# Performance work log

Measured on AMD Instinct MI355X. Metric: run time of the kernel, lower is better.

## Reference

```python
import math
import jax, jax.numpy as jnp
import numpy as np

NGRAM = 2
NUM_HEADS = 16
EMBED_DIM = 1024
HEAD_DIM = EMBED_DIM // NUM_HEADS
NUM_BUCKETS = 32
MAX_DIST = 128
REAL_T = 512
BSZ = 4
NEG = -10000.0


def _bucket_np(n):
    # unidirectional T5-style log bucket, matching _relative_positions_bucket
    n = np.maximum(n, 0)
    max_exact = NUM_BUCKETS // 2
    is_small = n < max_exact
    val = max_exact + np.log(np.maximum(n, 1) / max_exact) / math.log(MAX_DIST / max_exact) * (NUM_BUCKETS - max_exact)
    val = np.minimum(val, NUM_BUCKETS - 1).astype(np.int32)
    return np.where(is_small, n.astype(np.int32), val)


def setup_inputs() -> dict:
    key = jax.random.key(0)
    ks = jax.random.split(key, 4)
    T, B, E = REAL_T, BSZ, EMBED_DIM
    hidden_states = jax.random.normal(ks[0], ((1 + NGRAM) * T, B, E), jnp.float32)
    s = 1.0 / math.sqrt(E)  # ~xavier scale
    in_proj_weight = jax.random.uniform(ks[1], (3 * E, E), jnp.float32, -s, s)
    in_proj_bias = jnp.zeros((3 * E,), jnp.float32)
    rel_w = jax.random.uniform(ks[2], (NUM_BUCKETS * NUM_HEADS, E), jnp.float32, -s, s)
    rel_b = jnp.zeros((NUM_BUCKETS * NUM_HEADS,), jnp.float32)
    out_w = jax.random.uniform(ks[3], (E, E), jnp.float32, -s, s)
    out_b = jnp.zeros((E,), jnp.float32)
    # relative-position buckets (main stream: keys at positions 1..T)
    pos = np.arange(1, T + 1)
    i_buckets_main = np.broadcast_to(_bucket_np(pos[:, None] - pos[None, :]), (B, T, T)).copy()
    # predict stream keys: concat(main positions shifted by -1, predict positions)
    key_pos = np.concatenate([pos - 1, pos])
    i_buckets_ngram = np.broadcast_to(_bucket_np(pos[:, None] - key_pos[None, :]), (B, T, 2 * T)).copy()
    # masks
    t = np.arange(T)
    self_attn_mask = np.where(t[None, :] <= t[:, None], 0.0, NEG).astype(np.float32)  # causal [T,T]
    s_idx = np.arange(2 * T)
    allow = ((s_idx[None, :] < T) & (s_idx[None, :] <= t[:, None])) | (s_idx[None, :] == T + t[:, None])
    ngram_mask = np.broadcast_to(np.where(allow, 0.0, NEG).astype(np.float32), (NGRAM, T, 2 * T)).copy()
    return dict(
        hidden_states=hidden_states,
        in_proj_weight=in_proj_weight, in_proj_bias=in_proj_bias,
        rel_w=rel_w, rel_b=rel_b, out_w=out_w, out_b=out_b,
        self_attn_mask=jnp.asarray(self_attn_mask), ngram_mask=jnp.asarray(ngram_mask),
        i_buckets_main=jnp.asarray(i_buckets_main, jnp.int32),
        i_buckets_ngram=jnp.asarray(i_buckets_ngram, jnp.int32),
    )


def _rel_values(h, rel_w, rel_b):
    # h: [..., T, E] -> per-head bucket values [..., H, T, NUM_BUCKETS]
    vals = h @ rel_w.T + rel_b                              # [..., T, K*H]
    vals = vals.reshape(vals.shape[:-1] + (NUM_BUCKETS, NUM_HEADS))  # [..., T, K, H]
    return jnp.moveaxis(vals, (-1, -2), (-3, -1))           # [..., H, T, K]


def _forward(hidden_states, in_proj_weight, in_proj_bias, rel_w, rel_b, out_w, out_b,
             self_attn_mask, ngram_mask, i_buckets_main, i_buckets_ngram):
    tgt_len, B, E = hidden_states.shape
    T = tgt_len // (1 + NGRAM)
    H, d = NUM_HEADS, HEAD_DIM
    scaling = d ** -0.5

    qkv = hidden_states @ in_proj_weight.T + in_proj_bias
    q, k, v = jnp.split(qkv, 3, axis=-1)
    q = q * scaling

    def to_bh(x):  # [tgt_len, B, E] -> [B*H, tgt_len, d]
        return jnp.swapaxes(x.reshape(tgt_len, B * H, d), 0, 1)

    q, k, v = to_bh(q), to_bh(k), to_bh(v)
    q_main, k_main, v_main = q[:, :T], k[:, :T], v[:, :T]

    # ---- main stream ----
    aw_main = jnp.einsum('btd,bsd->bts', q_main, k_main)            # [BH,T,T]
    h_main = jnp.swapaxes(hidden_states[:T], 0, 1)                  # [B,T,E]
    vals_main = _rel_values(h_main, rel_w, rel_b)                   # [B,H,T,K]
    idx = jnp.broadcast_to(i_buckets_main[:, None], (B, H, T, T))
    rel_main = jnp.take_along_axis(vals_main, idx, axis=-1).reshape(B * H, T, T)
    aw_main = aw_main + rel_main + self_attn_mask[None]
    p_main = jax.nn.softmax(aw_main.astype(jnp.float32), axis=-1).astype(aw_main.dtype)
    attn_main = jnp.einsum('bts,bsd->btd', p_main, v_main)          # [BH,T,d]
    attn_main = jnp.swapaxes(attn_main, 0, 1).reshape(T, B, E) @ out_w.T + out_b

    # ---- ngram (predict) streams ----
    S2 = 2 * T
    q_ng = jnp.moveaxis(q[:, T:].reshape(B * H, NGRAM, T, d), 1, 0)  # [N,BH,T,d]
    k_ng = jnp.moveaxis(k[:, T:].reshape(B * H, NGRAM, T, d), 1, 0)
    v_ng = jnp.moveaxis(v[:, T:].reshape(B * H, NGRAM, T, d), 1, 0)
    k_cat = jnp.concatenate([jnp.broadcast_to(k_main[None], (NGRAM, B * H, T, d)), k_ng], axis=2)  # [N,BH,2T,d]
    v_cat = jnp.concatenate([jnp.broadcast_to(v_main[None], (NGRAM, B * H, T, d)), v_ng], axis=2)
    aw_ng = jnp.einsum('nbtd,nbsd->nbts', q_ng, k_cat)               # [N,BH,T,2T]
    h_ng = jnp.swapaxes(hidden_states[T:].reshape(NGRAM, T, B, E), 1, 2)  # [N,B,T,E]
    vals_ng = _rel_values(h_ng, rel_w, rel_b)                        # [N,B,H,T,K]
    idx2 = jnp.broadcast_to(i_buckets_ngram[None, :, None], (NGRAM, B, H, T, S2))
    rel_ng = jnp.take_along_axis(vals_ng, idx2, axis=-1).reshape(NGRAM, B * H, T, S2)
    aw_ng = aw_ng + rel_ng + ngram_mask[:, None]
    p_ng = jax.nn.softmax(aw_ng.astype(jnp.float32), axis=-1).astype(aw_ng.dtype)
    attn_ng = jnp.einsum('nbts,nbsd->nbtd', p_ng, v_cat)             # [N,BH,T,d]
    attn_ng = jnp.swapaxes(attn_ng, 1, 2).reshape(NGRAM, T, B, E) @ out_w.T + out_b

    return jnp.concatenate([attn_main, attn_ng.reshape(NGRAM * T, B, E)], axis=0)  # [(1+N)T,B,E]


def reference(hidden_states, in_proj_weight, in_proj_bias, rel_w, rel_b, out_w, out_b,
              self_attn_mask, ngram_mask, i_buckets_main, i_buckets_ngram):
    return _forward(hidden_states, in_proj_weight, in_proj_bias, rel_w, rel_b, out_w, out_b,
                    self_attn_mask, ngram_mask, i_buckets_main, i_buckets_ngram)
```

## Files before the change

kernel.cpp:

```cpp
#include <hip/hip_runtime.h>
#include <stdint.h>

#define T_LEN 512
#define NTOK  1536
#define EMB   1024
#define BS    4

typedef __bf16 bf16x8 __attribute__((ext_vector_type(8)));
typedef float  f32x4  __attribute__((ext_vector_type(4)));

__device__ __forceinline__ float bflo(unsigned short u){
  union { unsigned int i; float f; } a; a.i = ((unsigned int)u) << 16; return a.f;
}
__device__ __forceinline__ unsigned short f2bf(float f){
  union { float f; unsigned int i; } v; v.f = f;
  unsigned int x = v.i;
  return (unsigned short)((x + 0x7fffu + ((x >> 16) & 1u)) >> 16);
}

__device__ __forceinline__ void gld_lds16(const unsigned short* gptr, unsigned short* lptr){
  __builtin_amdgcn_global_load_lds(
      (const __attribute__((address_space(1))) unsigned int*)gptr,
      (__attribute__((address_space(3))) unsigned int*)lptr, 16, 0, 0);
}

__global__ __launch_bounds__(256)
void cast_k(const float* __restrict__ h, const float* __restrict__ wq,
            const float* __restrict__ rw, const float* __restrict__ ow,
            unsigned short* __restrict__ Hb, unsigned short* __restrict__ Wc,
            unsigned short* __restrict__ Ob)
{
  const size_t e = ((size_t)blockIdx.x * 256 + threadIdx.x) * 8;
  const float* src; unsigned short* dst;
  if (e < 6291456)            { src = h  + e;                 dst = Hb + e; }
  else if (e < 9437184)       { size_t o = e - 6291456;       src = wq + o; dst = Wc + o; }
  else if (e < 9961472)       { size_t o = e - 9437184;       src = rw + o; dst = Wc + 3145728 + o; }
  else                        { size_t o = e - 9961472;       src = ow + o; dst = Ob + o; }
  float4 f0 = *(const float4*)src, f1 = *(const float4*)(src + 4);
  unsigned short r[8];
  r[0]=f2bf(f0.x); r[1]=f2bf(f0.y); r[2]=f2bf(f0.z); r[3]=f2bf(f0.w);
  r[4]=f2bf(f1.x); r[5]=f2bf(f1.y); r[6]=f2bf(f1.z); r[7]=f2bf(f1.w);
  *(uint4*)dst = *(const uint4*)r;
}

template<int MODE>
__global__ __launch_bounds__(256)
void mgemm(const unsigned short* __restrict__ A,
           const unsigned short* __restrict__ W,
           const float* __restrict__ B0,
           const float* __restrict__ B1,
           unsigned short* __restrict__ Qo, unsigned short* __restrict__ Ko,
           unsigned short* __restrict__ Vo, float* __restrict__ VALS,
           float* __restrict__ OUT)
{
  constexpr int TM = (MODE == 0) ? 128 : 64;
  constexpr int NI = (MODE == 0) ? 4 : 2;
  __shared__ __align__(16) unsigned short SM[(TM + 128) * 32];
  unsigned short* As = SM;
  unsigned short* Bs = SM + TM*32;
  const int K = 1024;
  const int m0 = blockIdx.y * TM, n0 = blockIdx.x * 128;
  const int tid = threadIdx.x;
  const int wid = tid >> 6, lane = tid & 63;
  const int l15 = lane & 15, q8 = (lane >> 4) * 8;
  const int srow = lane >> 2, schunk = (lane & 3) * 8;
  const int wcol = (MODE == 0) ? (wid >> 1) * 64 : wid * 32;
  const int wtok = (MODE == 0) ? (wid & 1) * 64 : 0;

  f32x4 acc[NI][4];
  #pragma unroll
  for (int i=0;i<NI;i++)
    #pragma unroll
    for (int j=0;j<4;j++)
      #pragma unroll
      for (int r=0;r<4;r++) acc[i][j][r] = 0.f;

  for (int k0 = 0; k0 < K; k0 += 32) {
    if (MODE == 0) {
      #pragma unroll
      for (int p = 0; p < 2; ++p) {
        const int r0 = p*64 + wid*16;
        gld_lds16(A + (size_t)(m0 + r0 + srow)*K + k0 + schunk, &As[r0*32]);
      }
    } else {
      const int r0 = wid*16;
      gld_lds16(A + (size_t)(m0 + r0 + srow)*K + k0 + schunk, &As[r0*32]);
    }
    #pragma unroll
    for (int p = 0; p < 2; ++p) {
      const int r0 = p*64 + wid*16;
      gld_lds16(W + (size_t)(n0 + r0 + srow)*K + k0 + schunk, &Bs[r0*32]);
    }
    __syncthreads();
    bf16x8 wf[NI], hf[4];
    #pragma unroll
    for (int i=0;i<NI;i++) wf[i] = *(const bf16x8*)&Bs[(wcol + i*16 + l15)*32 + q8];
    #pragma unroll
    for (int j=0;j<4;j++)  hf[j] = *(const bf16x8*)&As[(wtok + j*16 + l15)*32 + q8];
    #pragma unroll
    for (int i=0;i<NI;i++)
      #pragma unroll
      for (int j=0;j<4;j++)
        acc[i][j] = __builtin_amdgcn_mfma_f32_16x16x32_bf16(wf[i], hf[j], acc[i][j], 0, 0, 0);
    __syncthreads();
  }
  const int rbase = (lane >> 4) * 4;

  if (MODE == 1) {
    #pragma unroll
    for (int i=0;i<NI;i++){
      const int c0l = wcol + i*16 + rbase;
      float4 b4 = *(const float4*)&B0[n0 + c0l];
      #pragma unroll
      for (int j=0;j<4;j++){
        const int tokrow = m0 + j*16 + l15;
        float4 st; st.x=acc[i][j][0]+b4.x; st.y=acc[i][j][1]+b4.y;
        st.z=acc[i][j][2]+b4.z; st.w=acc[i][j][3]+b4.w;
        *(float4*)&OUT[(size_t)tokrow*EMB + n0 + c0l] = st;
      }
    }
    return;
  }

  if (n0 < 2048) {
    const float sc = (n0 < 1024) ? 0.125f : 1.0f;
    unsigned short* base = (n0 < 1024) ? Qo : Ko;
    #pragma unroll
    for (int i=0;i<4;i++){
      const int cg = n0 + wcol + i*16 + rbase;
      const int hh = (cg & 1023) >> 6;
      const int d0 = cg & 63;
      float4 b4 = *(const float4*)&B0[cg];
      #pragma unroll
      for (int j=0;j<4;j++){
        const int tokrow = m0 + wtok + j*16 + l15;
        const int tok = tokrow >> 2, bb2 = tokrow & 3;
        unsigned short pk[4];
        pk[0]=f2bf((acc[i][j][0]+b4.x)*sc); pk[1]=f2bf((acc[i][j][1]+b4.y)*sc);
        pk[2]=f2bf((acc[i][j][2]+b4.z)*sc); pk[3]=f2bf((acc[i][j][3]+b4.w)*sc);
        *(uint2*)&base[((size_t)(bb2*16+hh)*NTOK + tok)*64 + d0] = *(const uint2*)pk;
      }
    }
  } else if (n0 < 3072) {
    unsigned short* Ts = SM;
    const int tok0 = m0 >> 2;
    #pragma unroll
    for (int ch=0; ch<2; ++ch){
      const int hh = ((n0 + ch*64) & 1023) >> 6;
      #pragma unroll
      for (int dh=0; dh<2; ++dh){
        if ((wid >> 1) == ch){
          #pragma unroll
          for (int ii=0; ii<2; ++ii){
            const int i = dh*2 + ii;
            const int cg = n0 + ch*64 + i*16 + rbase;
            float4 b4 = *(const float4*)&B0[cg];
            #pragma unroll
            for (int j=0;j<4;j++){
              const int trl = wtok + j*16 + l15;
              const int tokl = trl >> 2, bb2 = trl & 3;
              #pragma unroll
              for (int r=0;r<4;r++)
                Ts[(ii*16 + rbase + r)*160 + bb2*40 + tokl]
                  = f2bf(acc[i][j][r] + ((const float*)&b4)[r]);
            }
          }
        }
        __syncthreads();
        {
          const int unit = tid >> 1;
          const int dl = unit >> 2, bb2 = unit & 3, th = tid & 1;
          unsigned short* dst = Vo + ((size_t)(bb2*16+hh)*64 + dh*32 + dl)*NTOK
                                   + tok0 + th*16;
          const unsigned short* s = &Ts[dl*160 + bb2*40 + th*16];
          *(uint4*)dst       = *(const uint4*)s;
          *(uint4*)(dst + 8) = *(const uint4*)(s + 8);
        }
        __syncthreads();
      }
    }
  } else {
    float* Tsf = (float*)SM;
    const int tok0 = m0 >> 2;
    #pragma unroll
    for (int ch=0; ch<2; ++ch){
      #pragma unroll
      for (int i=0;i<4;i++){
        const int e2base = (n0 - 3072) + ch*64 + i*16;
        if ((wid >> 1) == ch){
          const int cg = n0 + ch*64 + i*16 + rbase;
          float4 b4 = *(const float4*)&B1[cg - 3072];
          #pragma unroll
          for (int j=0;j<4;j++){
            const int trl = wtok + j*16 + l15;
            const int tokl = trl >> 2, bb2 = trl & 3;
            #pragma unroll
            for (int r=0;r<4;r++)
              Tsf[(rbase + r)*144 + bb2*36 + tokl]
                = acc[i][j][r] + ((const float*)&b4)[r];
          }
        }
        __syncthreads();
        {
          const int pair = tid >> 2, tseg = (tid & 3) * 8;
          const int c = pair >> 2, bb2 = pair & 3;
          const int nb = e2base >> 4;
          float* dst = VALS + ((size_t)(bb2*32+nb)*16 + c)*NTOK + tok0 + tseg;
          const float* s = &Tsf[c*144 + bb2*36 + tseg];
          *(float4*)dst       = *(const float4*)s;
          *(float4*)(dst + 4) = *(const float4*)(s + 4);
        }
        __syncthreads();
      }
    }
  }
}

__global__ __launch_bounds__(256, 2)
void fattn(const unsigned short* __restrict__ Q,
           const unsigned short* __restrict__ K,
           const unsigned short* __restrict__ VT,
           const float* __restrict__ VALS,
           const int* __restrict__ IBM,
           const int* __restrict__ IBN,
           unsigned short* __restrict__ OUT)
{
  __shared__ float vls[3][64*33];
  __shared__ unsigned short Pl[4][16*72];
  __shared__ int fs[513];
  __shared__ float pex[4][16];
  __shared__ float lar[4][16];

  const int blk = blockIdx.x;
  const int half = blk >> 8, idx = blk & 255;
  const int pr = idx & 3, bh = idx >> 2;
  const int qt = half ? (7 - pr) : pr;
  const int tid = threadIdx.x, wid = tid >> 6, lane = tid & 63;
  const int l15 = lane & 15, q4 = lane >> 4;

  fs[tid]       = IBM[(size_t)tid * T_LEN];
  fs[tid + 256] = IBM[(size_t)(tid + 256) * T_LEN];
  if (tid == 0) fs[512] = IBN[(size_t)511 * (2*T_LEN)];

  int tokbase[3];
  #pragma unroll
  for (int c=0;c<3;c++) tokbase[c] = c*T_LEN + qt*64;

  {
    const int nb = tid >> 3, t8 = (tid & 7) * 8;
    const float* vr = VALS + ((size_t)((bh >> 4)*32 + nb)*16 + (bh & 15))*NTOK;
    #pragma unroll
    for (int c=0;c<3;c++){
      float4 a = *(const float4*)(vr + tokbase[c] + t8);
      float4 b = *(const float4*)(vr + tokbase[c] + t8 + 4);
      vls[c][(t8+0)*33 + nb] = a.x; vls[c][(t8+1)*33 + nb] = a.y;
      vls[c][(t8+2)*33 + nb] = a.z; vls[c][(t8+3)*33 + nb] = a.w;
      vls[c][(t8+4)*33 + nb] = b.x; vls[c][(t8+5)*33 + nb] = b.y;
      vls[c][(t8+6)*33 + nb] = b.z; vls[c][(t8+7)*33 + nb] = b.w;
    }
  }

  const unsigned short* Kbh = K  + (size_t)bh*NTOK*64;
  const unsigned short* Vbh = VT + (size_t)bh*64*NTOK;
  const int t = qt*64 + wid*16 + l15;

  bf16x8 bq[3][2];
  #pragma unroll
  for (int c=0;c<3;c++){
    const unsigned short* qp = Q + ((size_t)bh*NTOK + tokbase[c] + wid*16 + l15)*64 + q4*8;
    bq[c][0] = *(const bf16x8*)qp;
    bq[c][1] = *(const bf16x8*)(qp + 32);
  }

  f32x4 o[3][4];
  float lr[3];
  #pragma unroll
  for (int c=0;c<3;c++){
    lr[c] = 0.f;
    #pragma unroll
    for (int jd=0;jd<4;jd++)
      #pragma unroll
      for (int r=0;r<4;r++) o[c][jd][r] = 0.f;
  }
  const f32x4 zero = {0.f,0.f,0.f,0.f};
  unsigned short* Pw = &Pl[wid][0];

  __syncthreads();

  for (int tile = 0; tile <= qt; ++tile) {
    const int u0 = tile * 64;
    bf16x8 ka0[4], ka1[4], vb0[4], vb1[4];
    #pragma unroll
    for (int i=0;i<4;i++){
      const unsigned short* kp = Kbh + (size_t)(u0 + 16*i + l15)*64 + q4*8;
      ka0[i] = *(const bf16x8*)kp;  ka1[i] = *(const bf16x8*)(kp + 32);
      const unsigned short* vp = Vbh + (size_t)(16*i + l15)*NTOK + u0 + q4*8;
      vb0[i] = *(const bf16x8*)vp;  vb1[i] = *(const bf16x8*)(vp + 32);
    }
    #pragma unroll
    for (int c=0;c<3;c++){
      const int relofs = (c >= 1) ? 1 : 0;
      f32x4 st[4];
      #pragma unroll
      for (int i=0;i<4;i++){
        st[i] = __builtin_amdgcn_mfma_f32_16x16x32_bf16(ka0[i], bq[c][0], zero, 0, 0, 0);
        st[i] = __builtin_amdgcn_mfma_f32_16x16x32_bf16(ka1[i], bq[c][1], st[i], 0, 0, 0);
      }
      float lp = 0.f;
      #pragma unroll
      for (int i=0;i<4;i++){
        unsigned short pr4[4];
        #pragma unroll
        for (int r=0;r<4;r++){
          const int u = u0 + 16*i + q4*4 + r;
          const bool ok = (u <= t);
          const int nd = ok ? (t - u + relofs) : 0;
          const float rel = vls[c][(wid*16 + l15)*33 + fs[nd]];
          float p = ok ? __expf(st[i][r] + rel) : 0.f;
          const unsigned short pb = f2bf(p);
          pr4[r] = pb;
          lp += bflo(pb);
        }
        uint2 pk;
        pk.x = (unsigned int)pr4[0] | ((unsigned int)pr4[1] << 16);
        pk.y = (unsigned int)pr4[2] | ((unsigned int)pr4[3] << 16);
        *(uint2*)&Pw[l15*72 + 16*i + q4*4] = pk;
      }
      lp += __shfl_xor(lp, 16);
      lp += __shfl_xor(lp, 32);
      lr[c] += lp;
      bf16x8 ap0 = *(const bf16x8*)&Pw[l15*72 + q4*8];
      bf16x8 ap1 = *(const bf16x8*)&Pw[l15*72 + 32 + q4*8];
      #pragma unroll
      for (int jd=0;jd<4;jd++){
        o[c][jd] = __builtin_amdgcn_mfma_f32_16x16x32_bf16(ap0, vb0[jd], o[c][jd], 0, 0, 0);
        o[c][jd] = __builtin_amdgcn_mfma_f32_16x16x32_bf16(ap1, vb1[jd], o[c][jd], 0, 0, 0);
      }
    }
  }

  #pragma unroll
  for (int c=1;c<3;c++){
    const int qtok = tokbase[c] + wid*16 + l15;
    const unsigned short* qp2 = Q + ((size_t)bh*NTOK + qtok)*64 + q4*16;
    const unsigned short* kp2 = Kbh + (size_t)qtok*64 + q4*16;
    float s = 0.f;
    #pragma unroll
    for (int cc=0;cc<2;cc++){
      bf16x8 qv = *(const bf16x8*)(qp2 + cc*8);
      bf16x8 kv = *(const bf16x8*)(kp2 + cc*8);
      #pragma unroll
      for (int e=0;e<8;e++) s += (float)qv[e] * (float)kv[e];
    }
    s += __shfl_xor(s, 16);
    s += __shfl_xor(s, 32);
    const float p = __expf(s + vls[c][(wid*16 + l15)*33 + fs[0]]);
    lr[c] += p;
    pex[wid][l15] = p;
    #pragma unroll
    for (int r=0;r<4;r++){
      const int qloc = q4*4 + r;
      const float pq = pex[wid][qloc];
      const int qtk = tokbase[c] + wid*16 + qloc;
      #pragma unroll
      for (int jd=0;jd<4;jd++){
        const float vv = bflo(Vbh[(size_t)(16*jd + l15)*NTOK + qtk]);
        o[c][jd][r] += pq * vv;
      }
    }
  }

  const int b = bh >> 4, h = bh & 15;
  #pragma unroll
  for (int c=0;c<3;c++){
    lar[wid][l15] = lr[c];
    #pragma unroll
    for (int r=0;r<4;r++){
      const int qloc = q4*4 + r;
      const float inv = 1.0f / lar[wid][qloc];
      const int qtk = tokbase[c] + wid*16 + qloc;
      unsigned short* orow = OUT + ((size_t)qtk*BS + b)*EMB + h*64 + l15;
      #pragma unroll
      for (int jd=0;jd<4;jd++)
        orow[16*jd] = f2bf(o[c][jd][r] * inv);
    }
  }
}

extern "C" void kernel_launch(void* const* d_in, const int* in_sizes, int n_in,
                              void* d_out, int out_size, void* d_ws, size_t ws_size,
                              hipStream_t stream) {
  (void)in_sizes; (void)n_in; (void)out_size; (void)ws_size;
  const float* hidden = (const float*)d_in[0];
  const float* wqkv   = (const float*)d_in[1];
  const float* bqkv   = (const float*)d_in[2];
  const float* relw   = (const float*)d_in[3];
  const float* relb   = (const float*)d_in[4];
  const float* outw   = (const float*)d_in[5];
  const float* outb   = (const float*)d_in[6];
  const int* ibm = (const int*)d_in[9];
  const int* ibn = (const int*)d_in[10];

  unsigned short* Hb  = (unsigned short*)d_ws;
  unsigned short* Wc  = Hb + (size_t)6291456;
  unsigned short* Ob  = Wc + (size_t)3670016;
  unsigned short* Qb  = Ob + (size_t)1048576;
  unsigned short* Kb  = Qb + (size_t)6291456;
  unsigned short* VTb = Kb + (size_t)6291456;
  float* VLS = (float*)(VTb + (size_t)6291456);
  unsigned short* ATTb = Hb;

  cast_k<<<5376, 256, 0, stream>>>(hidden, wqkv, relw, outw, Hb, Wc, Ob);
  mgemm<0><<<dim3(28, 48), 256, 0, stream>>>(Hb, Wc, bqkv, relb,
                                             Qb, Kb, VTb, VLS, nullptr);
  fattn<<<512, 256, 0, stream>>>(Qb, Kb, VTb, VLS, ibm, ibn, ATTb);
  mgemm<1><<<dim3(8, 96), 256, 0, stream>>>(ATTb, Ob, outb, nullptr,
                                            nullptr, nullptr, nullptr, nullptr,
                                            (float*)d_out);
}
```

Before: 263.8 us.

## Load GEMM fragments directly from global memory, dropping LDS staging and barriers

The projection GEMM no longer stages A and W tiles through shared memory with async global-to-LDS loads and two barriers per k-step. Each wave now loads its MFMA operand fragments straight from global memory through per-row pointers, relying on L1/L2 for reuse. The output GEMM uses the same 128-row tile as the QKV GEMM, which halves its grid, and launch bounds now request two blocks per CU. This removes synchronisation and LDS traffic, but each operand is fetched by several waves without sharing, and the 16-byte-per-lane strided loads may cost more cache bandwidth and latency.

Result: slower. 406.0 us (+53.9%).

```diff
diff --git a/kernel.cpp b/kernel.cpp
--- a/kernel.cpp
+++ b/kernel.cpp
@@ -16,12 +16,6 @@
   union { float f; unsigned int i; } v; v.f = f;
   unsigned int x = v.i;
   return (unsigned short)((x + 0x7fffu + ((x >> 16) & 1u)) >> 16);
-}
-
-__device__ __forceinline__ void gld_lds16(const unsigned short* gptr, unsigned short* lptr){
-  __builtin_amdgcn_global_load_lds(
-      (const __attribute__((address_space(1))) unsigned int*)gptr,
-      (__attribute__((address_space(3))) unsigned int*)lptr, 16, 0, 0);
 }
 
 __global__ __launch_bounds__(256)
@@ -44,7 +38,7 @@
 }
 
 template<int MODE>
-__global__ __launch_bounds__(256)
+__global__ __launch_bounds__(256, 2)
 void mgemm(const unsigned short* __restrict__ A,
            const unsigned short* __restrict__ W,
            const float* __restrict__ B0,
@@ -53,67 +47,53 @@
            unsigned short* __restrict__ Vo, float* __restrict__ VALS,
            float* __restrict__ OUT)
 {
-  constexpr int TM = (MODE == 0) ? 128 : 64;
-  constexpr int NI = (MODE == 0) ? 4 : 2;
-  __shared__ __align__(16) unsigned short SM[(TM + 128) * 32];
-  unsigned short* As = SM;
-  unsigned short* Bs = SM + TM*32;
+  __shared__ __align__(16) unsigned short Ts[5120];
   const int K = 1024;
-  const int m0 = blockIdx.y * TM, n0 = blockIdx.x * 128;
+  const int m0 = blockIdx.y * 128, n0 = blockIdx.x * 128;
   const int tid = threadIdx.x;
   const int wid = tid >> 6, lane = tid & 63;
   const int l15 = lane & 15, q8 = (lane >> 4) * 8;
-  const int srow = lane >> 2, schunk = (lane & 3) * 8;
-  const int wcol = (MODE == 0) ? (wid >> 1) * 64 : wid * 32;
-  const int wtok = (MODE == 0) ? (wid & 1) * 64 : 0;
-
-  f32x4 acc[NI][4];
-  #pragma unroll
-  for (int i=0;i<NI;i++)
+  const int wcol = (wid >> 1) * 64;
+  const int wtok = (wid & 1) * 64;
+
+  const unsigned short* wp[4];
+  const unsigned short* ap[4];
+  #pragma unroll
+  for (int i=0;i<4;i++) wp[i] = W + (size_t)(n0 + wcol + i*16 + l15)*K + q8;
+  #pragma unroll
+  for (int j=0;j<4;j++) ap[j] = A + (size_t)(m0 + wtok + j*16 + l15)*K + q8;
+
+  f32x4 acc[4][4];
+  #pragma unroll
+  for (int i=0;i<4;i++)
     #pragma unroll
     for (int j=0;j<4;j++)
       #pragma unroll
       for (int r=0;r<4;r++) acc[i][j][r] = 0.f;
 
+  #pragma unroll 2
   for (int k0 = 0; k0 < K; k0 += 32) {
-    if (MODE == 0) {
-      #pragma unroll
-      for (int p = 0; p < 2; ++p) {
-        const int r0 = p*64 + wid*16;
-        gld_lds16(A + (size_t)(m0 + r0 + srow)*K + k0 + schunk, &As[r0*32]);
-      }
-    } else {
-      const int r0 = wid*16;
-      gld_lds16(A + (size_t)(m0 + r0 + srow)*K + k0 + schunk, &As[r0*32]);
-    }
-    #pragma unroll
-    for (int p = 0; p < 2; ++p) {
-      const int r0 = p*64 + wid*16;
-      gld_lds16(W + (size_t)(n0 + r0 + srow)*K + k0 + schunk, &Bs[r0*32]);
-    }
-    __syncthreads();
-    bf16x8 wf[NI], hf[4];
-    #pragma unroll
-    for (int i=0;i<NI;i++) wf[i] = *(const bf16x8*)&Bs[(wcol + i*16 + l15)*32 + q8];
-    #pragma unroll
-    for (int j=0;j<4;j++)  hf[j] = *(const bf16x8*)&As[(wtok + j*16 + l15)*32 + q8];
-    #pragma unroll
-    for (int i=0;i<NI;i++)
+    bf16x8 wf[4], hf[4];
+    #pragma unroll
+    for (int i=0;i<4;i++) wf[i] = *(const bf16x8*)(wp[i] + k0);
+    #pragma unroll
+    for (int j=0;j<4;j++) hf[j] = *(const bf16x8*)(ap[j] + k0);
+    #pragma unroll
+    for (int i=0;i<4;i++)
       #pragma unroll
       for (int j=0;j<4;j++)
         acc[i][j] = __builtin_amdgcn_mfma_f32_16x16x32_bf16(wf[i], hf[j], acc[i][j], 0, 0, 0);
-    __syncthreads();
   }
   const int rbase = (lane >> 4) * 4;
 
   if (MODE == 1) {
     #pragma unroll
-    for (int i=0;i<NI;i++){
+    for (int i=0;i<4;i++){
       const int c0l = wcol + i*16 + rbase;
       float4 b4 = *(const float4*)&B0[n0 + c0l];
       #pragma unroll
       for (int j=0;j<4;j++){
-        const int tokrow = m0 + j*16 + l15;
+        const int tokrow = m0 + wtok + j*16 + l15;
         float4 st; st.x=acc[i][j][0]+b4.x; st.y=acc[i][j][1]+b4.y;
         st.z=acc[i][j][2]+b4.z; st.w=acc[i][j][3]+b4.w;
         *(float4*)&OUT[(size_t)tokrow*EMB + n0 + c0l] = st;
@@ -142,7 +122,6 @@
       }
     }
   } else if (n0 < 3072) {
-    unsigned short* Ts = SM;
     const int tok0 = m0 >> 2;
     #pragma unroll
     for (int ch=0; ch<2; ++ch){
@@ -180,7 +159,7 @@
       }
     }
   } else {
-    float* Tsf = (float*)SM;
+    float* Tsf = (float*)Ts;
     const int tok0 = m0 >> 2;
     #pragma unroll
     for (int ch=0; ch<2; ++ch){
@@ -414,7 +393,7 @@
   mgemm<0><<<dim3(28, 48), 256, 0, stream>>>(Hb, Wc, bqkv, relb,
                                              Qb, Kb, VTb, VLS, nullptr);
   fattn<<<512, 256, 0, stream>>>(Qb, Kb, VTb, VLS, ibm, ibn, ATTb);
-  mgemm<1><<<dim3(8, 96), 256, 0, stream>>>(ATTb, Ob, outb, nullptr,
+  mgemm<1><<<dim3(8, 48), 256, 0, stream>>>(ATTb, Ob, outb, nullptr,
                                             nullptr, nullptr, nullptr, nullptr,
                                             (float*)d_out);
 }
```
